# Kernel tuning notes

Measured on AMD Instinct MI355X. Metric: run time of the kernel, lower is better.

Reference implementation:

```python
import jax, jax.numpy as jnp
import numpy as np

B, T = 128, 100
NOISE_STD = 0.1  # deterministic=False path

def leaky(x, slope):
    return jnp.where(x >= 0, x, slope * x)

def setup_inputs() -> dict:
    key = jax.random.key(0)
    ks = jax.random.split(key, 24)
    s = 0.02
    d = {}
    d["input_data"] = jax.random.normal(ks[0], (B, T, 3, 3), jnp.float32)
    d["eps"] = jax.random.normal(ks[1], (B, 64), jnp.float32)
    d["noise_eps"] = jax.random.normal(ks[2], (T, B, 4), jnp.float32)
    d["proj_W"] = jax.random.normal(ks[3], (4096, 9), jnp.float32) * s
    d["proj_b"] = jnp.zeros((4096,), jnp.float32)
    d["lstm_Wih"] = jax.random.normal(ks[4], (512, 4096), jnp.float32) * s
    d["lstm_Whh"] = jax.random.normal(ks[5], (512, 128), jnp.float32) * s
    d["lstm_bih"] = jnp.zeros((512,), jnp.float32)
    d["lstm_bhh"] = jnp.zeros((512,), jnp.float32)
    d["mu_W"] = jax.random.normal(ks[6], (64, 128), jnp.float32) * s
    d["mu_b"] = jnp.zeros((64,), jnp.float32)
    d["lv_W"] = jax.random.normal(ks[7], (64, 128), jnp.float32) * s
    d["lv_b"] = jnp.zeros((64,), jnp.float32)
    d["fcin_W"] = jax.random.normal(ks[8], (256, 64), jnp.float32) * s
    d["fcin_b"] = jnp.zeros((256,), jnp.float32)
    d["gru_Wih"] = jax.random.normal(ks[9], (783, 261), jnp.float32) * s
    d["gru_Whh"] = jax.random.normal(ks[10], (783, 261), jnp.float32) * s
    d["gru_bih"] = jnp.zeros((783,), jnp.float32)
    d["gru_bhh"] = jnp.zeros((783,), jnp.float32)
    d["jf_W1"] = jax.random.normal(ks[11], (64, 261), jnp.float32) * s
    d["jf_b1"] = jnp.zeros((64,), jnp.float32)
    d["jf_W2"] = jax.random.normal(ks[12], (9, 64), jnp.float32) * s
    d["jf_b2"] = jnp.zeros((9,), jnp.float32)
    return d

def reference(input_data, eps, noise_eps, proj_W, proj_b, lstm_Wih, lstm_Whh,
              lstm_bih, lstm_bhh, mu_W, mu_b, lv_W, lv_b, fcin_W, fcin_b,
              gru_Wih, gru_Whh, gru_bih, gru_bhh, jf_W1, jf_b1, jf_W2, jf_b2):
    b, t = input_data.shape[0], input_data.shape[1]
    pose = input_data.reshape(b, t, 9)
    # pose_projection: Linear(9, 4096) + LeakyReLU(0.1)
    proj = leaky(jnp.einsum('btj,kj->btk', pose, proj_W) + proj_b, 0.1)  # (B,T,4096)

    # LSTM over time, take final hidden state. PyTorch gate order: i,f,g,o.
    # Precompute input projections for all steps.
    x_gates = jnp.einsum('btk,gk->tbg', proj, lstm_Wih) + lstm_bih + lstm_bhh  # (T,B,512)
    hdim = 128
    def lstm_step(carry, xg):
        h, c = carry
        g = xg + h @ lstm_Whh.T  # (B,512)
        i, f, gg, o = jnp.split(g, 4, axis=-1)
        i, f, o = jax.nn.sigmoid(i), jax.nn.sigmoid(f), jax.nn.sigmoid(o)
        c = f * c + i * jnp.tanh(gg)
        h = o * jnp.tanh(c)
        return (h, c), None
    h0 = jnp.zeros((b, hdim), proj.dtype)
    (h_T, _), _ = jax.lax.scan(lstm_step, (h0, h0), x_gates)

    # VAE head (dropout in eval mode = identity)
    mu = leaky(h_T @ mu_W.T + mu_b, 0.1)
    logvar = jnp.clip(leaky(h_T @ lv_W.T + lv_b, 0.1), -10.0, 10.0)
    std = jnp.exp(0.5 * logvar)
    embedding = mu + eps * std

    x = embedding @ fcin_W.T + fcin_b  # (B,256)

    # Decoder GRU loop. PyTorch gate order: r,z,n; h' = (1-z)*n + z*h.
    noise = noise_eps * NOISE_STD  # (T,B,4)
    time_steps = (jnp.arange(t, dtype=x.dtype) / (t - 1))[:, None, None] * jnp.ones((t, b, 1), x.dtype)
    inp_seq = jnp.concatenate([jnp.broadcast_to(x[None], (t, b, 256)), noise, time_steps], axis=-1)  # (T,B,261)
    gx_seq = jnp.einsum('tbk,gk->tbg', inp_seq, gru_Wih) + gru_bih  # (T,B,783)

    def gru_step(h, gx):
        gh = h @ gru_Whh.T + gru_bhh
        gx_r, gx_z, gx_n = jnp.split(gx, 3, axis=-1)
        gh_r, gh_z, gh_n = jnp.split(gh, 3, axis=-1)
        r = jax.nn.sigmoid(gx_r + gh_r)
        z = jax.nn.sigmoid(gx_z + gh_z)
        n = jnp.tanh(gx_n + r * gh_n)
        h = (1.0 - z) * n + z * h
        frame = jax.nn.sigmoid(leaky(h @ jf_W1.T + jf_b1, 0.2) @ jf_W2.T + jf_b2)
        return h, frame

    h0g = jnp.zeros((b, 261), x.dtype)
    _, frames = jax.lax.scan(gru_step, h0g, gx_seq)  # (T,B,9)
    outputs = frames.transpose(1, 0, 2).reshape(b, t, 3, 3)
    return outputs, mu, logvar
```

## Files before the change

kernel.cpp:

```cpp
#include <hip/hip_runtime.h>
#include <hip/hip_bf16.h>

typedef float f32x4 __attribute__((ext_vector_type(4)));
typedef short s16x8 __attribute__((ext_vector_type(8)));

__device__ __forceinline__ float pv_sigm(float x){ return 1.0f/(1.0f + __expf(-x)); }
__device__ __forceinline__ float pv_tanh(float x){ float e = __expf(2.0f*x); return 1.0f - 2.0f/(e + 1.0f); }

__device__ __forceinline__ unsigned short pv_f2b(float x){
  union { float f; unsigned u; } c; c.f = x;
  unsigned r = (c.u + 0x7fffu + ((c.u >> 16) & 1u)) >> 16;
  return (unsigned short)r;
}
__device__ __forceinline__ unsigned pv_pack2(float a, float b){
  return ((unsigned)pv_f2b(b) << 16) | (unsigned)pv_f2b(a);
}
__device__ __forceinline__ float pv_lo(unsigned u){
  union { unsigned u; float f; } c; c.u = u << 16; return c.f;
}
__device__ __forceinline__ float pv_hi(unsigned u){
  union { unsigned u; float f; } c; c.u = u & 0xffff0000u; return c.f;
}

__device__ __forceinline__ unsigned char pv_fp8(float x){
  union { float f; unsigned u; } c; c.f = x;
  unsigned s = (c.u >> 24) & 0x80u;
  unsigned au = c.u & 0x7fffffffu;
  if (au == 0u) return (unsigned char)s;
  int ex = (int)(au >> 23) - 127;
  if (ex < -6) ex = -6;
  union { unsigned u; float f; } iv; iv.u = (unsigned)(3 - ex + 127) << 23;
  union { unsigned u; float f; } a;  a.u = au;
  int q = (int)rintf(a.f * iv.f);
  if (q >= 16) { q >>= 1; ex += 1; }
  unsigned bits;
  if (ex == -6 && q < 8) bits = (unsigned)q;
  else bits = (unsigned)(((ex + 7) << 3) | (q - 8));
  return (unsigned char)(s | bits);
}

#if defined(__has_builtin)
#if __has_builtin(__builtin_amdgcn_cvt_pk_fp8_f32)
#define PV_HW_FP8 1
#endif
#endif
__device__ __forceinline__ unsigned char pv_fp8_fast(float x){
#ifdef PV_HW_FP8
  return (unsigned char)__builtin_amdgcn_cvt_pk_fp8_f32(x, x, 0, false);
#else
  return pv_fp8(x);
#endif
}

__global__ void pv_prep_gru8(const float* Whh, const float* Wih,
                             unsigned long long* wfp8){
  int idx = blockIdx.x*256 + threadIdx.x;
  if (idx >= 28224) return;
  int T = idx / 576;
  int rem = idx - T*576;
  int c = rem >> 6;
  int l = rem & 63;
  int n = T*16 + (l & 15);
  int quad = l >> 4;
  unsigned long long v = 0ull;
  #pragma unroll
  for (int e = 0; e < 8; ++e) {
    int k = c*32 + quad*8 + e;
    float w = 0.0f;
    if (n < 783) {
      if (k < 261) w = Whh[n*261 + k];
      else if (k < 266 && n < 522) w = Wih[n*261 + 256 + (k - 261)];
    }
    v |= (unsigned long long)pv_fp8(8.0f*w) << (8*e);
  }
  wfp8[idx] = v;
}

__global__ __launch_bounds__(256) void pv_prep_wih(
    const float* __restrict__ Wih, unsigned* __restrict__ wihb)
{
  const int idx = blockIdx.x*256 + threadIdx.x;
  if (idx >= 262144) return;
  const float* src = Wih + idx*8;
  float4 a = *(const float4*)(src);
  float4 b = *(const float4*)(src + 4);
  uint4 o;
  o.x = pv_pack2(a.x, a.y);
  o.y = pv_pack2(a.z, a.w);
  o.z = pv_pack2(b.x, b.y);
  o.w = pv_pack2(b.z, b.w);
  *(uint4*)(wihb + idx*4) = o;
}

__global__ __launch_bounds__(512, 2) void pv_gemm3(
    const float* __restrict__ pose, const float* __restrict__ projW,
    const float* __restrict__ projb, const unsigned* __restrict__ wihb,
    const float* __restrict__ bih, const float* __restrict__ bhh,
    float* __restrict__ xg)
{
  __shared__ __align__(16) unsigned As2[128*20];
  __shared__ __align__(16) unsigned Bs2[2][512*20];
  __shared__ __align__(16) float Ws2[2][320];

  const int tid = threadIdx.x;
  const int m0 = blockIdx.x * 128;
  const int wave = tid >> 6, lane = tid & 63;
  const int wm = wave >> 2, wn = wave & 3;
  const int l16 = lane & 15, quad = lane >> 4;
  const int rl = tid >> 2, kq = tid & 3;

  float p[9];
  {
    const float* pr = pose + (m0 + rl)*9;
    #pragma unroll
    for (int j = 0; j < 9; ++j) p[j] = pr[j];
  }

  if (tid < 320) {
    Ws2[0][tid < 288 ? ((tid >> 5)*32 + (tid & 31)) : tid] =
        (tid < 288) ? projW[(tid & 31)*9 + (tid >> 5)] : projb[tid - 288];
  }
  #pragma unroll
  for (int i = 0; i < 4; ++i) {
    const int n = i*128 + rl;
    *(uint4*)(&Bs2[0][n*20 + kq*4]) = *(const uint4*)(wihb + n*2048 + kq*4);
  }
  __syncthreads();

  f32x4 acc[4][8];
  #pragma unroll
  for (int i = 0; i < 4; ++i)
    #pragma unroll
    for (int j = 0; j < 8; ++j) acc[i][j] = (f32x4){0.f,0.f,0.f,0.f};

  for (int kk = 0; kk < 128; ++kk) {
    const int cur = kk & 1, nxt = cur ^ 1;
    const int kn = kk + 1;

    uint4 bn0, bn1, bn2, bn3; float wv = 0.0f;
    if (kn < 128) {
      const unsigned* bsrc = wihb + kn*16 + kq*4;
      bn0 = *(const uint4*)(bsrc + (0*128 + rl)*2048);
      bn1 = *(const uint4*)(bsrc + (1*128 + rl)*2048);
      bn2 = *(const uint4*)(bsrc + (2*128 + rl)*2048);
      bn3 = *(const uint4*)(bsrc + (3*128 + rl)*2048);
      if (tid < 320)
        wv = (tid < 288) ? projW[kn*288 + (tid & 31)*9 + (tid >> 5)]
                         : projb[kn*32 + (tid - 288)];
    }

    {
      const float* W = Ws2[cur];
      f32x4 slo = *(const f32x4*)(W + 288 + kq*8);
      f32x4 shi = *(const f32x4*)(W + 292 + kq*8);
      #pragma unroll
      for (int j = 0; j < 9; ++j) {
        f32x4 wlo = *(const f32x4*)(W + j*32 + kq*8);
        f32x4 whi = *(const f32x4*)(W + j*32 + kq*8 + 4);
        slo += p[j]*wlo;
        shi += p[j]*whi;
      }
      #pragma unroll
      for (int e = 0; e < 4; ++e) {
        slo[e] = fmaxf(slo[e], 0.1f*slo[e]);
        shi[e] = fmaxf(shi[e], 0.1f*shi[e]);
      }
      uint4 av;
      av.x = pv_pack2(slo[0], slo[1]);
      av.y = pv_pack2(slo[2], slo[3]);
      av.z = pv_pack2(shi[0], shi[1]);
      av.w = pv_pack2(shi[2], shi[3]);
      *(uint4*)(&As2[rl*20 + kq*4]) = av;
    }

    if (kn < 128) {
      unsigned* bdst = &Bs2[nxt][rl*20 + kq*4];
      *(uint4*)(bdst + 0*128*20) = bn0;
      *(uint4*)(bdst + 1*128*20) = bn1;
      *(uint4*)(bdst + 2*128*20) = bn2;
      *(uint4*)(bdst + 3*128*20) = bn3;
      if (tid < 320)
        Ws2[nxt][tid < 288 ? ((tid >> 5)*32 + (tid & 31)) : tid] = wv;
    }
    __syncthreads();

    const unsigned short* As16 = (const unsigned short*)As2;
    const unsigned short* Bs16 = (const unsigned short*)Bs2[cur];
    s16x8 af[4];
    #pragma unroll
    for (int i = 0; i < 4; ++i)
      af[i] = *(const s16x8*)(As16 + (wm*64 + i*16 + l16)*40 + quad*8);
    #pragma unroll
    for (int j = 0; j < 8; ++j) {
      s16x8 bv = *(const s16x8*)(Bs16 + (wn*128 + j*16 + l16)*40 + quad*8);
      #pragma unroll
      for (int i = 0; i < 4; ++i)
        acc[i][j] = __builtin_amdgcn_mfma_f32_16x16x32_bf16(af[i], bv, acc[i][j], 0, 0, 0);
    }
    __syncthreads();
  }

  #pragma unroll
  for (int j = 0; j < 8; ++j) {
    int col = wn*128 + j*16 + l16;
    float bsum = bih[col] + bhh[col];
    #pragma unroll
    for (int i = 0; i < 4; ++i) {
      #pragma unroll
      for (int r = 0; r < 4; ++r) {
        int row = m0 + wm*64 + i*16 + quad*4 + r;
        int bb = row / 100;
        int tt = row - bb*100;
        xg[(tt*128 + bb)*512 + col] = acc[i][j][r] + bsum;
      }
    }
  }
}

__global__ __launch_bounds__(256) void pv_gemm(
    const float* pose, const float* projW, const float* projb,
    const float* Wih, const float* bih, const float* bhh,
    float* xg)
{
  __shared__ __align__(16) unsigned As[128*24];
  __shared__ __align__(16) unsigned Bs[128*24];
  __shared__ float Ws[320];

  const int tid = threadIdx.x;
  const int m0 = blockIdx.x * 128;
  const int n0 = blockIdx.y * 128;

  const int rl = tid >> 1;
  const int kh = tid & 1;
  float p0,p1,p2,p3,p4,p5,p6,p7,p8;
  {
    const float* pr = pose + (m0 + rl) * 9;
    p0=pr[0]; p1=pr[1]; p2=pr[2]; p3=pr[3]; p4=pr[4];
    p5=pr[5]; p6=pr[6]; p7=pr[7]; p8=pr[8];
  }

  const int wave = tid >> 6;
  const int lane = tid & 63;
  const int wm = wave >> 1, wn = wave & 1;
  const int l16 = lane & 15, quad = lane >> 4;

  f32x4 acc[4][4];
  #pragma unroll
  for (int i = 0; i < 4; ++i)
    #pragma unroll
    for (int j = 0; j < 4; ++j) acc[i][j] = (f32x4){0.f,0.f,0.f,0.f};

  for (int kk = 0; kk < 128; ++kk) {
    __syncthreads();
    for (int idx = tid; idx < 320; idx += 256)
      Ws[idx] = (idx < 288) ? projW[kk*288 + idx] : projb[kk*32 + (idx - 288)];
    #pragma unroll
    for (int i = 0; i < 8; ++i) {
      int q = tid + i*256;
      int nl = q >> 4;
      int kp = q & 15;
      const float* src = Wih + (n0 + nl)*4096 + kk*32 + kp*2;
      Bs[nl*24 + kp] = pv_pack2(src[0], src[1]);
    }
    __syncthreads();
    {
      const int kbase = kh*16;
      const float* wbase = Ws + kbase*9;
      float av[16];
      #pragma unroll
      for (int u = 0; u < 16; ++u) {
        const float* wr = wbase + u*9;
        float s = Ws[288 + kbase + u]
                + p0*wr[0] + p1*wr[1] + p2*wr[2] + p3*wr[3] + p4*wr[4]
                + p5*wr[5] + p6*wr[6] + p7*wr[7] + p8*wr[8];
        av[u] = fmaxf(s, 0.1f*s);
      }
      #pragma unroll
      for (int q = 0; q < 8; ++q)
        As[rl*24 + kh*8 + q] = pv_pack2(av[2*q], av[2*q+1]);
    }
    __syncthreads();
    const unsigned short* As16 = (const unsigned short*)As;
    const unsigned short* Bs16 = (const unsigned short*)Bs;
    s16x8 af[4], bfv[4];
    #pragma unroll
    for (int i = 0; i < 4; ++i)
      af[i] = *(const s16x8*)(As16 + (wm*64 + i*16 + l16)*48 + quad*8);
    #pragma unroll
    for (int j = 0; j < 4; ++j)
      bfv[j] = *(const s16x8*)(Bs16 + (wn*64 + j*16 + l16)*48 + quad*8);
    #pragma unroll
    for (int i = 0; i < 4; ++i)
      #pragma unroll
      for (int j = 0; j < 4; ++j)
        acc[i][j] = __builtin_amdgcn_mfma_f32_16x16x32_bf16(af[i], bfv[j], acc[i][j], 0, 0, 0);
  }
  #pragma unroll
  for (int j = 0; j < 4; ++j) {
    int col = n0 + wn*64 + j*16 + l16;
    float bsum = bih[col] + bhh[col];
    #pragma unroll
    for (int i = 0; i < 4; ++i) {
      #pragma unroll
      for (int r = 0; r < 4; ++r) {
        int row = m0 + wm*64 + i*16 + quad*4 + r;
        int bb = row / 100;
        int tt = row - bb*100;
        xg[(tt*128 + bb)*512 + col] = acc[i][j][r] + bsum;
      }
    }
  }
}

__global__ __attribute__((amdgpu_waves_per_eu(4, 4)))
__launch_bounds__(1024) void pv_lstm(
    const float* xg, const float* Whh, float* hT)
{
  __shared__ __align__(16) unsigned short Hs[16*136];
  __shared__ float Ds[16*544];
  const int tid = threadIdx.x;
  const int wv = tid >> 6;
  const int lane = tid & 63;
  const int l16 = lane & 15, quad = lane >> 4;
  const int m0 = blockIdx.x * 16;

  s16x8 bfr[2][4];
  #pragma unroll
  for (int tt = 0; tt < 2; ++tt) {
    const int g = (wv*2 + tt)*16 + l16;
    #pragma unroll
    for (int c = 0; c < 4; ++c) {
      s16x8 v;
      #pragma unroll
      for (int e = 0; e < 8; ++e)
        v[e] = (short)pv_f2b(Whh[g*128 + c*32 + quad*8 + e]);
      bfr[tt][c] = v;
    }
  }
  for (int i = tid; i < 16*136; i += 1024) Hs[i] = 0;
  float cst[2] = {0.0f, 0.0f};

  float xv[2][4];
  #pragma unroll
  for (int tt = 0; tt < 2; ++tt) {
    const int g = (wv*2 + tt)*16 + l16;
    #pragma unroll
    for (int r = 0; r < 4; ++r)
      xv[tt][r] = xg[(0*128 + m0 + quad*4 + r)*512 + g];
  }
  __syncthreads();

  for (int t = 0; t < 100; ++t) {
    float xn[2][4];
    if (t < 99) {
      #pragma unroll
      for (int tt = 0; tt < 2; ++tt) {
        const int g = (wv*2 + tt)*16 + l16;
        #pragma unroll
        for (int r = 0; r < 4; ++r)
          xn[tt][r] = xg[((t+1)*128 + m0 + quad*4 + r)*512 + g];
      }
    }
    f32x4 acc0 = {0,0,0,0}, acc1 = {0,0,0,0};
    #pragma unroll
    for (int c = 0; c < 4; ++c) {
      s16x8 a = *(const s16x8*)(Hs + l16*136 + c*32 + quad*8);
      acc0 = __builtin_amdgcn_mfma_f32_16x16x32_bf16(a, bfr[0][c], acc0, 0, 0, 0);
      acc1 = __builtin_amdgcn_mfma_f32_16x16x32_bf16(a, bfr[1][c], acc1, 0, 0, 0);
    }
    #pragma unroll
    for (int r = 0; r < 4; ++r) {
      Ds[(quad*4 + r)*544 + (wv*2 + 0)*16 + l16] = acc0[r] + xv[0][r];
      Ds[(quad*4 + r)*544 + (wv*2 + 1)*16 + l16] = acc1[r] + xv[1][r];
    }
    __syncthreads();
    #pragma unroll
    for (int e = 0; e < 2; ++e) {
      const int el = tid + e*1024;
      const int m = el >> 7, j = el & 127;
      float gi = Ds[m*544 + j];
      float gf = Ds[m*544 + 128 + j];
      float gg = Ds[m*544 + 256 + j];
      float go = Ds[m*544 + 384 + j];
      float c = pv_sigm(gf)*cst[e] + pv_sigm(gi)*pv_tanh(gg);
      cst[e] = c;
      float h = pv_sigm(go)*pv_tanh(c);
      Hs[m*136 + j] = pv_f2b(h);
      if (t == 99) hT[(m0 + m)*128 + j] = h;
    }
    __syncthreads();
    if (t < 99) {
      #pragma unroll
      for (int tt = 0; tt < 2; ++tt)
        #pragma unroll
        for (int r = 0; r < 4; ++r)
          xv[tt][r] = xn[tt][r];
    }
  }
}

__global__ __launch_bounds__(64) void pv_head(
    const float* hT, const float* eps,
    const float* muW, const float* mub,
    const float* lvW, const float* lvb,
    const float* fcW, const float* fcb,
    float* xvec, float* out)
{
  __shared__ float hrow[128];
  __shared__ float emb[64];
  const int b = blockIdx.x, j = threadIdx.x;
  hrow[j] = hT[b*128 + j];
  hrow[j + 64] = hT[b*128 + 64 + j];
  __syncthreads();
  float sm = mub[j], sl = lvb[j];
  for (int k = 0; k < 128; ++k) {
    sm += hrow[k]*muW[j*128 + k];
    sl += hrow[k]*lvW[j*128 + k];
  }
  float mu = fmaxf(sm, 0.1f*sm);
  float lv = fmaxf(sl, 0.1f*sl);
  lv = fminf(fmaxf(lv, -10.0f), 10.0f);
  float em = mu + eps[b*64 + j]*__expf(0.5f*lv);
  emb[j] = em;
  out[115200 + b*64 + j] = mu;
  out[123392 + b*64 + j] = lv;
  __syncthreads();
  for (int c4 = 0; c4 < 4; ++c4) {
    int c = c4*64 + j;
    float s = fcb[c];
    for (int k = 0; k < 64; ++k) s += emb[k]*fcW[c*64 + k];
    xvec[b*256 + c] = s;
  }
}

__global__ __launch_bounds__(256) void pv_gxbase(
    const float* xvec, const float* Wih,
    const float* bih, const float* bhh, float* gxb)
{
  __shared__ float xs[8*256];
  const int tid = threadIdx.x;
  const int bg = blockIdx.x;
  const int gg = blockIdx.y;
  for (int i = tid; i < 2048; i += 256) xs[i] = xvec[bg*2048 + i];
  __syncthreads();
  const int g = gg*256 + tid;
  if (g >= 783) return;
  float bias = bih[g] + ((g < 522) ? bhh[g] : 0.0f);
  float a0=bias,a1=bias,a2=bias,a3=bias,a4=bias,a5=bias,a6=bias,a7=bias;
  const float* wr = Wih + g*261;
  for (int k = 0; k < 256; ++k) {
    float w = wr[k];
    a0 += xs[0*256 + k]*w; a1 += xs[1*256 + k]*w;
    a2 += xs[2*256 + k]*w; a3 += xs[3*256 + k]*w;
    a4 += xs[4*256 + k]*w; a5 += xs[5*256 + k]*w;
    a6 += xs[6*256 + k]*w; a7 += xs[7*256 + k]*w;
  }
  gxb[(bg*8 + 0)*783 + g] = a0; gxb[(bg*8 + 1)*783 + g] = a1;
  gxb[(bg*8 + 2)*783 + g] = a2; gxb[(bg*8 + 3)*783 + g] = a3;
  gxb[(bg*8 + 4)*783 + g] = a4; gxb[(bg*8 + 5)*783 + g] = a5;
  gxb[(bg*8 + 6)*783 + g] = a6; gxb[(bg*8 + 7)*783 + g] = a7;
}

__global__ __attribute__((amdgpu_waves_per_eu(4, 4)))
__launch_bounds__(1024) void pv_gru(
    const float* gxb, const unsigned long long* wfp8, const float* Wih,
    const float* bhh, const float* noise, float* hseq)
{
  __shared__ __align__(16) unsigned char Afp8[16*296];
  __shared__ float Ds[4*788];
  const int tid = threadIdx.x;
  const int wv = tid >> 6;
  const int lane = tid & 63;
  const int l16 = lane & 15, quad = lane >> 4;
  const int m0 = blockIdx.x * 4;
  const int tbase = (wv < 15) ? wv*3 : 45;
  const int ntiles = (wv < 15) ? 3 : 4;

  long bfr[4][9];
  #pragma unroll
  for (int tt = 0; tt < 4; ++tt) {
    if (tt < ntiles) {
      #pragma unroll
      for (int c = 0; c < 9; ++c)
        bfr[tt][c] = (long)wfp8[((tbase + tt)*9 + c)*64 + lane];
    } else {
      #pragma unroll
      for (int c = 0; c < 9; ++c) bfr[tt][c] = 0;
    }
  }

  const int m_u = tid >> 8;
  const int j_u = tid & 255;
  const int sec = (j_u < 5);
  float wn0, wn1, wn2, wn3, wn4, bhhn, gxr, gxz, gxn;
  float wn0b=0, wn1b=0, wn2b=0, wn3b=0, wn4b=0, bhhnb=0, gxrb=0, gxzb=0, gxnb=0;
  {
    const float* wrow = Wih + (522 + j_u)*261 + 256;
    wn0 = 0.1f*wrow[0]; wn1 = 0.1f*wrow[1]; wn2 = 0.1f*wrow[2];
    wn3 = 0.1f*wrow[3]; wn4 = wrow[4];
    bhhn = bhh[522 + j_u];
    const float* gb = gxb + (m0 + m_u)*783;
    gxr = gb[j_u]; gxz = gb[261 + j_u]; gxn = gb[522 + j_u];
    if (sec) {
      const int j2 = 256 + j_u;
      const float* wrow2 = Wih + (522 + j2)*261 + 256;
      wn0b = 0.1f*wrow2[0]; wn1b = 0.1f*wrow2[1]; wn2b = 0.1f*wrow2[2];
      wn3b = 0.1f*wrow2[3]; wn4b = wrow2[4];
      bhhnb = bhh[522 + j2];
      gxrb = gb[j2]; gxzb = gb[261 + j2]; gxnb = gb[522 + j2];
    }
  }
  float* hptr = hseq + (m0 + m_u)*261 + j_u;
  const float* np = noise + (m0 + m_u)*4;
  float h1 = 0.0f, h2 = 0.0f;

  for (int i = tid; i < 16*296; i += 1024) Afp8[i] = 0;
  __syncthreads();
  if (tid < 20) {
    const int m = tid/5, i = tid - (tid/5)*5;
    float v = (i < 4) ? noise[(m0 + m)*4 + i]*0.1f : 0.0f;
    Afp8[m*296 + 261 + i] = pv_fp8(4.0f*v);
  }
  __syncthreads();

  const float inv32 = 1.0f/32.0f;
  for (int t = 0; t < 100; ++t) {
    f32x4 acc[4];
    #pragma unroll
    for (int tt = 0; tt < 4; ++tt) acc[tt] = (f32x4){0,0,0,0};
    #pragma unroll
    for (int c = 0; c < 9; ++c) {
      const long a = *(const long*)(Afp8 + l16*296 + c*32 + quad*8);
      #pragma unroll
      for (int tt = 0; tt < 4; ++tt)
        if (tt < ntiles)
          acc[tt] = __builtin_amdgcn_mfma_f32_16x16x32_fp8_fp8(a, bfr[tt][c], acc[tt], 0, 0, 0);
    }
    if (quad == 0) {
      #pragma unroll
      for (int tt = 0; tt < 4; ++tt)
        if (tt < ntiles) {
          const int n = (tbase + tt)*16 + l16;
          #pragma unroll
          for (int r = 0; r < 4; ++r)
            Ds[r*788 + n] = acc[tt][r];
        }
    }
    __syncthreads();
    {
      const float tv = (float)t * (1.0f/99.0f);
      const float4 ne = *(const float4*)np;
      {
        const float* dm = Ds + m_u*788;
        float Dr = dm[j_u]*inv32 + gxr;
        float Dz = dm[261 + j_u]*inv32 + gxz;
        float Dn = dm[522 + j_u]*inv32;
        float nterm = ne.x*wn0 + ne.y*wn1 + ne.z*wn2 + ne.w*wn3 + tv*wn4;
        float r_ = pv_sigm(Dr);
        float z_ = pv_sigm(Dz);
        float n_ = pv_tanh(gxn + nterm + r_*(Dn + bhhn));
        h1 = (1.0f - z_)*n_ + z_*h1;
        hptr[0] = h1;
        Afp8[m_u*296 + j_u] = pv_fp8_fast(4.0f*h1);
      }
      if (sec) {
        const int j2 = 256 + j_u;
        const float* dm = Ds + m_u*788;
        float Dr = dm[j2]*inv32 + gxrb;
        float Dz = dm[261 + j2]*inv32 + gxzb;
        float Dn = dm[522 + j2]*inv32;
        float nterm = ne.x*wn0b + ne.y*wn1b + ne.z*wn2b + ne.w*wn3b + tv*wn4b;
        float r_ = pv_sigm(Dr);
        float z_ = pv_sigm(Dz);
        float n_ = pv_tanh(gxnb + nterm + r_*(Dn + bhhnb));
        h2 = (1.0f - z_)*n_ + z_*h2;
        hptr[256] = h2;
        Afp8[m_u*296 + j2] = pv_fp8_fast(4.0f*h2);
      }
    }
    if (tid < 20 && t < 99) {
      const int m = tid/5, i = tid - (tid/5)*5;
      float v = (i < 4) ? noise[((t+1)*128 + m0 + m)*4 + i]*0.1f
                        : (t+1)*(1.0f/99.0f);
      Afp8[m*296 + 261 + i] = pv_fp8(4.0f*v);
    }
    hptr += 128*261;
    np += 512;
    __syncthreads();
  }
}

__global__ __launch_bounds__(256) void pv_frames(
    const float* hseq, const float* W1, const float* b1,
    const float* W2, const float* b2, float* out)
{
  __shared__ __align__(16) float h16[16*264];
  __shared__ unsigned w1p[64*133];
  __shared__ float f1s[16*66];
  __shared__ float w2s[576];
  const int tid = threadIdx.x;
  const int r0 = blockIdx.x * 16;
  for (int i = tid; i < 16*264; i += 256) {
    int r = i / 264, k = i - r*264;
    h16[i] = (k < 261) ? hseq[(r0 + r)*261 + k] : 0.0f;
  }
  for (int i = tid; i < 64*131; i += 256) {
    int c = i/131, kp = i - (i/131)*131;
    int k = kp*2;
    float a0 = W1[c*261 + k];
    float a1 = (k + 1 < 261) ? W1[c*261 + k + 1] : 0.0f;
    w1p[c*133 + kp] = pv_pack2(a0, a1);
  }
  for (int i = tid; i < 576; i += 256) w2s[i] = W2[i];
  __syncthreads();
  #pragma unroll
  for (int e = 0; e < 4; ++e) {
    const int el = tid + e*256;
    const int r = el >> 6, c = el & 63;
    float s = b1[c];
    const unsigned* wp = w1p + c*133;
    const float* hr = h16 + r*264;
    for (int kp = 0; kp < 131; ++kp) {
      unsigned w = wp[kp];
      s += pv_lo(w)*hr[2*kp] + pv_hi(w)*hr[2*kp + 1];
    }
    f1s[r*66 + c] = fmaxf(s, 0.2f*s);
  }
  __syncthreads();
  if (tid < 144) {
    const int r = tid/9, oc = tid - (tid/9)*9;
    float s = b2[oc];
    const float* fr = f1s + r*66;
    const float* w = w2s + oc*64;
    #pragma unroll 8
    for (int k = 0; k < 64; ++k) s += fr[k]*w[k];
    const int rt = r0 + r;
    const int tt = rt >> 7, bb = rt & 127;
    out[bb*900 + tt*9 + oc] = pv_sigm(s);
  }
}

extern "C" __attribute__((visibility("default")))
void kernel_launch(void* const* d_in, const int* in_sizes, int n_in,
                   void* d_out, int out_size, void* d_ws, size_t ws_size,
                   hipStream_t stream)
{
  (void)in_sizes; (void)n_in; (void)out_size;
  const float* input_data = (const float*)d_in[0];
  const float* eps        = (const float*)d_in[1];
  const float* noise_eps  = (const float*)d_in[2];
  const float* proj_W     = (const float*)d_in[3];
  const float* proj_b     = (const float*)d_in[4];
  const float* lstm_Wih   = (const float*)d_in[5];
  const float* lstm_Whh   = (const float*)d_in[6];
  const float* lstm_bih   = (const float*)d_in[7];
  const float* lstm_bhh   = (const float*)d_in[8];
  const float* mu_W       = (const float*)d_in[9];
  const float* mu_b       = (const float*)d_in[10];
  const float* lv_W       = (const float*)d_in[11];
  const float* lv_b       = (const float*)d_in[12];
  const float* fcin_W     = (const float*)d_in[13];
  const float* fcin_b     = (const float*)d_in[14];
  const float* gru_Wih    = (const float*)d_in[15];
  const float* gru_Whh    = (const float*)d_in[16];
  const float* gru_bih    = (const float*)d_in[17];
  const float* gru_bhh    = (const float*)d_in[18];
  const float* jf_W1      = (const float*)d_in[19];
  const float* jf_b1      = (const float*)d_in[20];
  const float* jf_W2      = (const float*)d_in[21];
  const float* jf_b2      = (const float*)d_in[22];

  char* w = (char*)d_ws;
  float*              xg   = (float*)(w);
  unsigned long long* wfp8 = (unsigned long long*)(w + 26214400);
  float*              hT   = (float*)(w + 26440192);
  float*              xvec = (float*)(w + 26505728);
  float*              gxb  = (float*)(w + 26636800);
  float*              hseq = (float*)(w + 27037696);
  unsigned*           wihb = (unsigned*)(w + 40400896);
  float*              outf = (float*)d_out;

  const int use_split = (ws_size >= (size_t)44595200ull);

  pv_prep_gru8<<<111, 256, 0, stream>>>(gru_Whh, gru_Wih, wfp8);
  if (use_split) {
    pv_prep_wih<<<1024, 256, 0, stream>>>(lstm_Wih, wihb);
    pv_gemm3<<<100, 512, 0, stream>>>(input_data, proj_W, proj_b, wihb,
                                      lstm_bih, lstm_bhh, xg);
  } else {
    pv_gemm<<<dim3(100, 4), 256, 0, stream>>>(input_data, proj_W, proj_b,
                                              lstm_Wih, lstm_bih, lstm_bhh, xg);
  }
  pv_lstm<<<8, 1024, 0, stream>>>(xg, lstm_Whh, hT);
  pv_head<<<128, 64, 0, stream>>>(hT, eps, mu_W, mu_b, lv_W, lv_b,
                                  fcin_W, fcin_b, xvec, outf);
  pv_gxbase<<<dim3(16, 4), 256, 0, stream>>>(xvec, gru_Wih, gru_bih, gru_bhh, gxb);
  pv_gru<<<32, 1024, 0, stream>>>(gxb, wfp8, gru_Wih, gru_bhh, noise_eps, hseq);
  pv_frames<<<800, 256, 0, stream>>>(hseq, jf_W1, jf_b1, jf_W2, jf_b2, outf);
}
```

Baseline: 836.7 us.

## Reorganize LSTM and GRU recurrences so each wave owns all gates, double-buffer state

The LSTM and GRU weight tiles are remapped so each wave holds the r/z/n (or i/f/g/o) gate columns for the same hidden units. Gate nonlinearities can then run directly on MFMA accumulators without a shared-memory scatter and a second barrier per step. The hidden-state operand is double-buffered in LDS so a single __syncthreads per timestep suffices, and GRU noise is preloaded into LDS. The LSTM now uses 512 threads with more registers per wave, and the GRU elementwise work is concentrated on quad-0 lanes, which could serialize that tail.

New measurement: 1.438 ms. +71.9%, slower.

```diff
diff --git a/kernel.cpp b/kernel.cpp
--- a/kernel.cpp
+++ b/kernel.cpp
@@ -55,21 +55,25 @@
 __global__ void pv_prep_gru8(const float* Whh, const float* Wih,
                              unsigned long long* wfp8){
   int idx = blockIdx.x*256 + threadIdx.x;
-  if (idx >= 28224) return;
+  if (idx >= 29376) return;
   int T = idx / 576;
   int rem = idx - T*576;
   int c = rem >> 6;
   int l = rem & 63;
-  int n = T*16 + (l & 15);
+  int l16 = l & 15;
   int quad = l >> 4;
+  int jb = T / 3;
+  int ty = T - jb*3;
+  int j = jb*16 + l16;
+  int g = ty*261 + j;
   unsigned long long v = 0ull;
   #pragma unroll
   for (int e = 0; e < 8; ++e) {
     int k = c*32 + quad*8 + e;
     float w = 0.0f;
-    if (n < 783) {
-      if (k < 261) w = Whh[n*261 + k];
-      else if (k < 266 && n < 522) w = Wih[n*261 + 256 + (k - 261)];
+    if (j < 261) {
+      if (k < 261) w = Whh[g*261 + k];
+      else if (k < 266 && ty < 2) w = Wih[g*261 + 256 + (k - 261)];
     }
     v |= (unsigned long long)pv_fp8(8.0f*w) << (8*e);
   }
@@ -312,90 +316,84 @@
   }
 }
 
-__global__ __attribute__((amdgpu_waves_per_eu(4, 4)))
-__launch_bounds__(1024) void pv_lstm(
-    const float* xg, const float* Whh, float* hT)
-{
-  __shared__ __align__(16) unsigned short Hs[16*136];
-  __shared__ float Ds[16*544];
+__global__ __launch_bounds__(512) void pv_lstm2(
+    const float* __restrict__ xg, const float* __restrict__ Whh,
+    float* __restrict__ hT)
+{
+  __shared__ __align__(16) unsigned short Hs2[2][16*136];
   const int tid = threadIdx.x;
   const int wv = tid >> 6;
   const int lane = tid & 63;
   const int l16 = lane & 15, quad = lane >> 4;
   const int m0 = blockIdx.x * 16;
-
-  s16x8 bfr[2][4];
-  #pragma unroll
-  for (int tt = 0; tt < 2; ++tt) {
-    const int g = (wv*2 + tt)*16 + l16;
+  const int j = wv*16 + l16;
+
+  s16x8 bfr[4][4];
+  #pragma unroll
+  for (int ty = 0; ty < 4; ++ty) {
+    const int g = ty*128 + j;
     #pragma unroll
     for (int c = 0; c < 4; ++c) {
       s16x8 v;
       #pragma unroll
       for (int e = 0; e < 8; ++e)
         v[e] = (short)pv_f2b(Whh[g*128 + c*32 + quad*8 + e]);
-      bfr[tt][c] = v;
-    }
-  }
-  for (int i = tid; i < 16*136; i += 1024) Hs[i] = 0;
-  float cst[2] = {0.0f, 0.0f};
-
-  float xv[2][4];
-  #pragma unroll
-  for (int tt = 0; tt < 2; ++tt) {
-    const int g = (wv*2 + tt)*16 + l16;
-    #pragma unroll
-    for (int r = 0; r < 4; ++r)
-      xv[tt][r] = xg[(0*128 + m0 + quad*4 + r)*512 + g];
-  }
+      bfr[ty][c] = v;
+    }
+  }
+  for (int i = tid; i < 2*16*136; i += 512) ((unsigned short*)Hs2)[i] = 0;
+
+  float cst[4] = {0.f, 0.f, 0.f, 0.f};
+  const float* xbase = xg + (m0 + quad*4)*512 + j;
+
+  float xv[4][4];
+  #pragma unroll
+  for (int r = 0; r < 4; ++r)
+    #pragma unroll
+    for (int ty = 0; ty < 4; ++ty)
+      xv[r][ty] = xbase[(0*128 + r)*512 + ty*128];
   __syncthreads();
 
   for (int t = 0; t < 100; ++t) {
-    float xn[2][4];
+    const int cur = t & 1, nxt = cur ^ 1;
+    float xn[4][4];
     if (t < 99) {
       #pragma unroll
-      for (int tt = 0; tt < 2; ++tt) {
-        const int g = (wv*2 + tt)*16 + l16;
+      for (int r = 0; r < 4; ++r)
         #pragma unroll
-        for (int r = 0; r < 4; ++r)
-          xn[tt][r] = xg[((t+1)*128 + m0 + quad*4 + r)*512 + g];
-      }
-    }
-    f32x4 acc0 = {0,0,0,0}, acc1 = {0,0,0,0};
+        for (int ty = 0; ty < 4; ++ty)
+          xn[r][ty] = xbase[((t+1)*128 + r)*512 + ty*128];
+    }
+    f32x4 acc[4];
+    #pragma unroll
+    for (int ty = 0; ty < 4; ++ty) acc[ty] = (f32x4){0.f,0.f,0.f,0.f};
     #pragma unroll
     for (int c = 0; c < 4; ++c) {
-      s16x8 a = *(const s16x8*)(Hs + l16*136 + c*32 + quad*8);
-      acc0 = __builtin_amdgcn_mfma_f32_16x16x32_bf16(a, bfr[0][c], acc0, 0, 0, 0);
-      acc1 = __builtin_amdgcn_mfma_f32_16x16x32_bf16(a, bfr[1][c], acc1, 0, 0, 0);
+      s16x8 a = *(const s16x8*)(&Hs2[cur][l16*136 + c*32 + quad*8]);
+      #pragma unroll
+      for (int ty = 0; ty < 4; ++ty)
+        acc[ty] = __builtin_amdgcn_mfma_f32_16x16x32_bf16(a, bfr[ty][c], acc[ty], 0, 0, 0);
     }
     #pragma unroll
     for (int r = 0; r < 4; ++r) {
-      Ds[(quad*4 + r)*544 + (wv*2 + 0)*16 + l16] = acc0[r] + xv[0][r];
-      Ds[(quad*4 + r)*544 + (wv*2 + 1)*16 + l16] = acc1[r] + xv[1][r];
+      float gi = acc[0][r] + xv[r][0];
+      float gf = acc[1][r] + xv[r][1];
+      float gg = acc[2][r] + xv[r][2];
+      float go = acc[3][r] + xv[r][3];
+      float c_ = pv_sigm(gf)*cst[r] + pv_sigm(gi)*pv_tanh(gg);
+      cst[r] = c_;
+      float h = pv_sigm(go)*pv_tanh(c_);
+      Hs2[nxt][(quad*4 + r)*136 + j] = pv_f2b(h);
+      if (t == 99) hT[(m0 + quad*4 + r)*128 + j] = h;
+    }
+    if (t < 99) {
+      #pragma unroll
+      for (int r = 0; r < 4; ++r)
+        #pragma unroll
+        for (int ty = 0; ty < 4; ++ty)
+          xv[r][ty] = xn[r][ty];
     }
     __syncthreads();
-    #pragma unroll
-    for (int e = 0; e < 2; ++e) {
-      const int el = tid + e*1024;
-      const int m = el >> 7, j = el & 127;
-      float gi = Ds[m*544 + j];
-      float gf = Ds[m*544 + 128 + j];
-      float gg = Ds[m*544 + 256 + j];
-      float go = Ds[m*544 + 384 + j];
-      float c = pv_sigm(gf)*cst[e] + pv_sigm(gi)*pv_tanh(gg);
-      cst[e] = c;
-      float h = pv_sigm(go)*pv_tanh(c);
-      Hs[m*136 + j] = pv_f2b(h);
-      if (t == 99) hT[(m0 + m)*128 + j] = h;
-    }
-    __syncthreads();
-    if (t < 99) {
-      #pragma unroll
-      for (int tt = 0; tt < 2; ++tt)
-        #pragma unroll
-        for (int r = 0; r < 4; ++r)
-          xv[tt][r] = xn[tt][r];
-    }
   }
 }
 
@@ -462,130 +460,139 @@
 }
 
 __global__ __attribute__((amdgpu_waves_per_eu(4, 4)))
-__launch_bounds__(1024) void pv_gru(
-    const float* gxb, const unsigned long long* wfp8, const float* Wih,
-    const float* bhh, const float* noise, float* hseq)
-{
-  __shared__ __align__(16) unsigned char Afp8[16*296];
-  __shared__ float Ds[4*788];
+__launch_bounds__(1024) void pv_gru2(
+    const float* __restrict__ gxb, const unsigned long long* __restrict__ wfp8,
+    const float* __restrict__ Wih, const float* __restrict__ bhh,
+    const float* __restrict__ noise, float* __restrict__ hseq)
+{
+  __shared__ __align__(16) unsigned char A2[2][16*296];
+  __shared__ __align__(16) float ns[1600];
   const int tid = threadIdx.x;
   const int wv = tid >> 6;
   const int lane = tid & 63;
   const int l16 = lane & 15, quad = lane >> 4;
   const int m0 = blockIdx.x * 4;
-  const int tbase = (wv < 15) ? wv*3 : 45;
-  const int ntiles = (wv < 15) ? 3 : 4;
-
-  long bfr[4][9];
-  #pragma unroll
-  for (int tt = 0; tt < 4; ++tt) {
-    if (tt < ntiles) {
+  const int ntiles = (wv < 15) ? 3 : 6;
+
+  long bfr[6][9];
+  #pragma unroll
+  for (int u = 0; u < 6; ++u) {
+    if (u < ntiles) {
+      const int grp = (u < 3) ? wv : 16;
+      const int ty  = (u < 3) ? u : u - 3;
+      const int T = grp*3 + ty;
       #pragma unroll
       for (int c = 0; c < 9; ++c)
-        bfr[tt][c] = (long)wfp8[((tbase + tt)*9 + c)*64 + lane];
+        bfr[u][c] = (long)wfp8[(T*9 + c)*64 + lane];
     } else {
       #pragma unroll
-      for (int c = 0; c < 9; ++c) bfr[tt][c] = 0;
-    }
-  }
-
-  const int m_u = tid >> 8;
-  const int j_u = tid & 255;
-  const int sec = (j_u < 5);
-  float wn0, wn1, wn2, wn3, wn4, bhhn, gxr, gxz, gxn;
-  float wn0b=0, wn1b=0, wn2b=0, wn3b=0, wn4b=0, bhhnb=0, gxrb=0, gxzb=0, gxnb=0;
-  {
-    const float* wrow = Wih + (522 + j_u)*261 + 256;
-    wn0 = 0.1f*wrow[0]; wn1 = 0.1f*wrow[1]; wn2 = 0.1f*wrow[2];
-    wn3 = 0.1f*wrow[3]; wn4 = wrow[4];
-    bhhn = bhh[522 + j_u];
-    const float* gb = gxb + (m0 + m_u)*783;
-    gxr = gb[j_u]; gxz = gb[261 + j_u]; gxn = gb[522 + j_u];
-    if (sec) {
-      const int j2 = 256 + j_u;
-      const float* wrow2 = Wih + (522 + j2)*261 + 256;
-      wn0b = 0.1f*wrow2[0]; wn1b = 0.1f*wrow2[1]; wn2b = 0.1f*wrow2[2];
-      wn3b = 0.1f*wrow2[3]; wn4b = wrow2[4];
-      bhhnb = bhh[522 + j2];
-      gxrb = gb[j2]; gxzb = gb[261 + j2]; gxnb = gb[522 + j2];
-    }
-  }
-  float* hptr = hseq + (m0 + m_u)*261 + j_u;
-  const float* np = noise + (m0 + m_u)*4;
-  float h1 = 0.0f, h2 = 0.0f;
-
-  for (int i = tid; i < 16*296; i += 1024) Afp8[i] = 0;
+      for (int c = 0; c < 9; ++c) bfr[u][c] = 0;
+    }
+  }
+
+  const int j1 = wv*16 + l16;
+  const int j2 = 256 + l16;
+  const int up1 = (quad == 0);
+  const int up2 = (quad == 0) && (wv == 15) && (l16 < 5);
+  float wnA[5], bhhnA = 0.f, gxrA[4], gxzA[4], gxnA[4], hA[4];
+  float wnB[5], bhhnB = 0.f, gxrB[4], gxzB[4], gxnB[4], hB[4];
+  #pragma unroll
+  for (int r = 0; r < 4; ++r) { hA[r] = 0.f; hB[r] = 0.f; }
+  if (up1) {
+    const float* wrow = Wih + (522 + j1)*261 + 256;
+    wnA[0] = 0.1f*wrow[0]; wnA[1] = 0.1f*wrow[1]; wnA[2] = 0.1f*wrow[2];
+    wnA[3] = 0.1f*wrow[3]; wnA[4] = wrow[4];
+    bhhnA = bhh[522 + j1];
+    #pragma unroll
+    for (int r = 0; r < 4; ++r) {
+      const float* gb = gxb + (m0 + r)*783;
+      gxrA[r] = gb[j1]; gxzA[r] = gb[261 + j1]; gxnA[r] = gb[522 + j1];
+    }
+  }
+  if (up2) {
+    const float* wrow = Wih + (522 + j2)*261 + 256;
+    wnB[0] = 0.1f*wrow[0]; wnB[1] = 0.1f*wrow[1]; wnB[2] = 0.1f*wrow[2];
+    wnB[3] = 0.1f*wrow[3]; wnB[4] = wrow[4];
+    bhhnB = bhh[522 + j2];
+    #pragma unroll
+    for (int r = 0; r < 4; ++r) {
+      const float* gb = gxb + (m0 + r)*783;
+      gxrB[r] = gb[j2]; gxzB[r] = gb[261 + j2]; gxnB[r] = gb[522 + j2];
+    }
+  }
+
+  for (int i = tid; i < 2*16*296; i += 1024) ((unsigned char*)A2)[i] = 0;
+  for (int i = tid; i < 1600; i += 1024) {
+    const int t = i >> 4, m = (i >> 2) & 3, ii = i & 3;
+    ns[i] = noise[(t*128 + m0 + m)*4 + ii];
+  }
   __syncthreads();
   if (tid < 20) {
     const int m = tid/5, i = tid - (tid/5)*5;
     float v = (i < 4) ? noise[(m0 + m)*4 + i]*0.1f : 0.0f;
-    Afp8[m*296 + 261 + i] = pv_fp8(4.0f*v);
+    A2[0][m*296 + 261 + i] = pv_fp8(4.0f*v);
   }
   __syncthreads();
 
   const float inv32 = 1.0f/32.0f;
   for (int t = 0; t < 100; ++t) {
-    f32x4 acc[4];
-    #pragma unroll
-    for (int tt = 0; tt < 4; ++tt) acc[tt] = (f32x4){0,0,0,0};
+    const int cur = t & 1, nxt = cur ^ 1;
+    f32x4 acc[6];
+    #pragma unroll
+    for (int u = 0; u < 6; ++u) acc[u] = (f32x4){0,0,0,0};
     #pragma unroll
     for (int c = 0; c < 9; ++c) {
-      const long a = *(const long*)(Afp8 + l16*296 + c*32 + quad*8);
-      #pragma unroll
-      for (int tt = 0; tt < 4; ++tt)
-        if (tt < ntiles)
-          acc[tt] = __builtin_amdgcn_mfma_f32_16x16x32_fp8_fp8(a, bfr[tt][c], acc[tt], 0, 0, 0);
-    }
-    if (quad == 0) {
-      #pragma unroll
-      for (int tt = 0; tt < 4; ++tt)
-        if (tt < ntiles) {
-          const int n = (tbase + tt)*16 + l16;
-          #pragma unroll
-          for (int r = 0; r < 4; ++r)
-            Ds[r*788 + n] = acc[tt][r];
-        }
-    }
-    __syncthreads();
-    {
+      const long a = *(const long*)(&A2[cur][l16*296 + c*32 + quad*8]);
+      #pragma unroll
+      for (int u = 0; u < 6; ++u)
+        if (u < ntiles)
+          acc[u] = __builtin_amdgcn_mfma_f32_16x16x32_fp8_fp8(a, bfr[u][c], acc[u], 0, 0, 0);
+    }
+
+    if (up1) {
       const float tv = (float)t * (1.0f/99.0f);
-      const float4 ne = *(const float4*)np;
-      {
-        const float* dm = Ds + m_u*788;
-        float Dr = dm[j_u]*inv32 + gxr;
-        float Dz = dm[261 + j_u]*inv32 + gxz;
-        float Dn = dm[522 + j_u]*inv32;
-        float nterm = ne.x*wn0 + ne.y*wn1 + ne.z*wn2 + ne.w*wn3 + tv*wn4;
+      float4 nem[4];
+      #pragma unroll
+      for (int r = 0; r < 4; ++r)
+        nem[r] = *(const float4*)(&ns[t*16 + r*4]);
+      #pragma unroll
+      for (int r = 0; r < 4; ++r) {
+        float Dr = acc[0][r]*inv32 + gxrA[r];
+        float Dz = acc[1][r]*inv32 + gxzA[r];
+        float Dn = acc[2][r]*inv32;
+        float nterm = nem[r].x*wnA[0] + nem[r].y*wnA[1] + nem[r].z*wnA[2]
+                    + nem[r].w*wnA[3] + tv*wnA[4];
         float r_ = pv_sigm(Dr);
         float z_ = pv_sigm(Dz);
-        float n_ = pv_tanh(gxn + nterm + r_*(Dn + bhhn));
-        h1 = (1.0f - z_)*n_ + z_*h1;
-        hptr[0] = h1;
-        Afp8[m_u*296 + j_u] = pv_fp8_fast(4.0f*h1);
+        float n_ = pv_tanh(gxnA[r] + nterm + r_*(Dn + bhhnA));
+        hA[r] = (1.0f - z_)*n_ + z_*hA[r];
+        hseq[(t*128 + m0 + r)*261 + j1] = hA[r];
+        A2[nxt][r*296 + j1] = pv_fp8_fast(4.0f*hA[r]);
       }
-      if (sec) {
-        const int j2 = 256 + j_u;
-        const float* dm = Ds + m_u*788;
-        float Dr = dm[j2]*inv32 + gxrb;
-        float Dz = dm[261 + j2]*inv32 + gxzb;
-        float Dn = dm[522 + j2]*inv32;
-        float nterm = ne.x*wn0b + ne.y*wn1b + ne.z*wn2b + ne.w*wn3b + tv*wn4b;
-        float r_ = pv_sigm(Dr);
-        float z_ = pv_sigm(Dz);
-        float n_ = pv_tanh(gxnb + nterm + r_*(Dn + bhhnb));
-        h2 = (1.0f - z_)*n_ + z_*h2;
-        hptr[256] = h2;
-        Afp8[m_u*296 + j2] = pv_fp8_fast(4.0f*h2);
+      if (up2) {
+        #pragma unroll
+        for (int r = 0; r < 4; ++r) {
+          float Dr = acc[3][r]*inv32 + gxrB[r];
+          float Dz = acc[4][r]*inv32 + gxzB[r];
+          float Dn = acc[5][r]*inv32;
+          float nterm = nem[r].x*wnB[0] + nem[r].y*wnB[1] + nem[r].z*wnB[2]
+                      + nem[r].w*wnB[3] + tv*wnB[4];
+          float r_ = pv_sigm(Dr);
+          float z_ = pv_sigm(Dz);
+          float n_ = pv_tanh(gxnB[r] + nterm + r_*(Dn + bhhnB));
+          hB[r] = (1.0f - z_)*n_ + z_*hB[r];
+          hseq[(t*128 + m0 + r)*261 + j2] = hB[r];
+          A2[nxt][r*296 + j2] = pv_fp8_fast(4.0f*hB[r]);
+        }
       }
     }
-    if (tid < 20 && t < 99) {
-      const int m = tid/5, i = tid - (tid/5)*5;
-      float v = (i < 4) ? noise[((t+1)*128 + m0 + m)*4 + i]*0.1f
+    if (t < 99 && wv == 1 && lane >= 32 && lane < 52) {
+      const int k = lane - 32;
+      const int m = k/5, i = k - (k/5)*5;
+      float v = (i < 4) ? ns[(t+1)*16 + m*4 + i]*0.1f
                         : (t+1)*(1.0f/99.0f);
-      Afp8[m*296 + 261 + i] = pv_fp8(4.0f*v);
-    }
-    hptr += 128*261;
-    np += 512;
+      A2[nxt][m*296 + 261 + i] = pv_fp8(4.0f*v);
+    }
     __syncthreads();
   }
 }
@@ -673,16 +680,16 @@
   char* w = (char*)d_ws;
   float*              xg   = (float*)(w);
   unsigned long long* wfp8 = (unsigned long long*)(w + 26214400);
-  float*              hT   = (float*)(w + 26440192);
-  float*              xvec = (float*)(w + 26505728);
-  float*              gxb  = (float*)(w + 26636800);
-  float*              hseq = (float*)(w + 27037696);
-  unsigned*           wihb = (unsigned*)(w + 40400896);
+  float*              hT   = (float*)(w + 26449408);
+  float*              xvec = (float*)(w + 26514944);
+  float*              gxb  = (float*)(w + 26646016);
+  float*              hseq = (float*)(w + 27046912);
+  unsigned*           wihb = (unsigned*)(w + 40410112);
   float*              outf = (float*)d_out;
 
-  const int use_split = (ws_size >= (size_t)44595200ull);
-
-  pv_prep_gru8<<<111, 256, 0, stream>>>(gru_Whh, gru_Wih, wfp8);
+  const int use_split = (ws_size >= (size_t)44604416ull);
+
+  pv_prep_gru8<<<115, 256, 0, stream>>>(gru_Whh, gru_Wih, wfp8);
   if (use_split) {
     pv_prep_wih<<<1024, 256, 0, stream>>>(lstm_Wih, wihb);
     pv_gemm3<<<100, 512, 0, stream>>>(input_data, proj_W, proj_b, wihb,
@@ -691,10 +698,10 @@
     pv_gemm<<<dim3(100, 4), 256, 0, stream>>>(input_data, proj_W, proj_b,
                                               lstm_Wih, lstm_bih, lstm_bhh, xg);
   }
-  pv_lstm<<<8, 1024, 0, stream>>>(xg, lstm_Whh, hT);
+  pv_lstm2<<<8, 512, 0, stream>>>(xg, lstm_Whh, hT);
   pv_head<<<128, 64, 0, stream>>>(hT, eps, mu_W, mu_b, lv_W, lv_b,
                                   fcin_W, fcin_b, xvec, outf);
   pv_gxbase<<<dim3(16, 4), 256, 0, stream>>>(xvec, gru_Wih, gru_bih, gru_bhh, gxb);
-  pv_gru<<<32, 1024, 0, stream>>>(gxb, wfp8, gru_Wih, gru_bhh, noise_eps, hseq);
+  pv_gru2<<<32, 1024, 0, stream>>>(gxb, wfp8, gru_Wih, gru_bhh, noise_eps, hseq);
   pv_frames<<<800, 256, 0, stream>>>(hseq, jf_W1, jf_b1, jf_W2, jf_b2, outf);
 }
```
